# Kernel optimization log

Measured on AMD Instinct MI355X. Metric: run time of the kernel, lower is better.

Reference implementation:

```python
import jax, jax.numpy as jnp
import numpy as np

B, N, D = 8, 2048, 512


def setup_inputs() -> dict:
    key = jax.random.key(0)
    ks = jax.random.split(key, 8)
    s = 1.0 / np.sqrt(D)
    return {
        "x": jax.random.normal(ks[0], (B, N, D), dtype=jnp.float32),
        "event_lengths": jax.random.randint(ks[1], (B,), 1, N + 1, dtype=jnp.int64),
        "Wq": jax.random.uniform(ks[2], (D, D), jnp.float32, -s, s),
        "bq": jnp.zeros((D,), jnp.float32),
        "Wk": jax.random.uniform(ks[3], (D, D), jnp.float32, -s, s),
        "bk": jnp.zeros((D,), jnp.float32),
        "Wv": jax.random.uniform(ks[4], (D, D), jnp.float32, -s, s),
        "bv": jnp.zeros((D,), jnp.float32),
    }


def reference(x, event_lengths, Wq, bq, Wk, bk, Wv, bv):
    # x: [B, N, D]; linear layers follow torch convention y = x @ W^T + b
    q = jnp.einsum("bnd,ed->bne", x, Wq) + bq
    k = jnp.einsum("bnd,ed->bne", x, Wk) + bk
    v = jnp.einsum("bnd,ed->bne", x, Wv) + bv

    d = x.shape[-1]
    scores = jnp.einsum("bqd,bkd->bqk", q, k) / jnp.sqrt(jnp.asarray(d, jnp.float32))

    # per-sample padding mask: valid iff row < len AND col < len
    n = x.shape[1]
    idx = jnp.arange(n)
    L = event_lengths[:, None, None]  # [B,1,1]
    mask = (idx[None, :, None] < L) & (idx[None, None, :] < L)  # [B,N,N]
    scores = jnp.where(mask, scores, jnp.float32(-1e9))

    attn = jax.nn.softmax(scores, axis=-1)  # dropout omitted (eval mode)
    return jnp.einsum("bqk,bkd->bqd", attn, v)
```

## Files before the change

kernel.cpp:

```cpp
#include <hip/hip_runtime.h>

typedef _Float16 half8 __attribute__((ext_vector_type(8)));
typedef _Float16 half4 __attribute__((ext_vector_type(4)));
typedef float    floatx4 __attribute__((ext_vector_type(4)));
typedef float    float4v __attribute__((ext_vector_type(4)));

#define BB 8
#define NN 2048
#define DD 512


#define WAITV(N)  asm volatile("s_waitcnt vmcnt(" #N ")" ::: "memory")
#define WAITL0()  asm volatile("s_waitcnt lgkmcnt(0)" ::: "memory")
#define BARRIER() asm volatile("s_barrier" ::: "memory")

__device__ __forceinline__ void stage_tile(const _Float16* __restrict__ g,
                                           int gstride, _Float16* lds,
                                           int w, int lane)
{
#pragma unroll
    for (int j = 0; j < 2; ++j) {
        int grp = w * 2 + j;
        int r   = grp * 16 + (lane >> 2);
        int cb  = (lane & 3) ^ ((r >> 1) & 3);
        const _Float16* gp = g + (size_t)r * gstride + cb * 8;
        _Float16* lp = lds + grp * 512;
        __builtin_amdgcn_global_load_lds(
            (const __attribute__((address_space(1))) void*)gp,
            (__attribute__((address_space(3))) void*)lp, 16, 0, 0);
    }
}

__device__ __forceinline__ void stage_tile64(const _Float16* __restrict__ g,
                                             int gstride, _Float16* lds,
                                             int w, int lane)
{
    int r  = w * 16 + (lane >> 2);
    int cb = (lane & 3) ^ ((r >> 1) & 3);
    const _Float16* gp = g + (size_t)r * gstride + cb * 8;
    _Float16* lp = lds + w * 512;
    __builtin_amdgcn_global_load_lds(
        (const __attribute__((address_space(1))) void*)gp,
        (__attribute__((address_space(3))) void*)lp, 16, 0, 0);
}

__device__ __forceinline__ half8 frag(const _Float16* tile, int m, int quad)
{
    return *(const half8*)&tile[m * 32 + ((quad ^ ((m >> 1) & 3)) * 8)];
}

__global__ __launch_bounds__(256) void prep_kernel(
    const float* __restrict__ x, const float* __restrict__ Wq,
    const float* __restrict__ Wk, const float* __restrict__ Wv,
    const int* __restrict__ lens,
    _Float16* __restrict__ xh, _Float16* __restrict__ wqh,
    _Float16* __restrict__ wkh, _Float16* __restrict__ wvh)
{
    const int XQ = (BB * NN * DD) / 4;
    const int WQ = (DD * DD) / 4;
    int t = blockIdx.x * 256 + threadIdx.x;
    const float* src; _Float16* dst; int i;
    if (t < XQ) {
        int row = t >> 7;
        int b   = row >> 11;
        if ((row & 2047) >= ((lens[b] + 127) & ~127)) return;
        src = x;  dst = xh;  i = t;
    }
    else if (t < XQ + WQ)   { src = Wq; dst = wqh; i = t - XQ; }
    else if (t < XQ + 2*WQ) { src = Wk; dst = wkh; i = t - XQ - WQ; }
    else if (t < XQ + 3*WQ) { src = Wv; dst = wvh; i = t - XQ - 2*WQ; }
    else return;
    float4v f = *(const float4v*)&src[(size_t)i * 4];
    half4 h;
    for (int j = 0; j < 4; ++j) h[j] = (_Float16)f[j];
    *(half4*)&dst[(size_t)i * 4] = h;
}

__global__ __launch_bounds__(256) void meanx_kernel(
    const float* __restrict__ x, float* __restrict__ sx)
{
    const int b  = blockIdx.y;
    const int n0 = blockIdx.x * 64;
    const int d0 = threadIdx.x;
    float s0 = 0.f, s1 = 0.f;
    const float* base = x + ((size_t)b * NN + n0) * DD;
    for (int n = 0; n < 64; ++n) {
        s0 += base[n * DD + d0];
        s1 += base[n * DD + d0 + 256];
    }
    atomicAdd(&sx[b * DD + d0], s0);
    atomicAdd(&sx[b * DD + d0 + 256], s1);
}

__global__ __launch_bounds__(256) void mvgemv_kernel(
    const float* __restrict__ Wv, const float* __restrict__ bv,
    const float* __restrict__ sx, float* __restrict__ mean_v)
{
    const int blk = blockIdx.x;
    const int b   = blk >> 7;
    const int e   = (blk & 127) * 4 + (threadIdx.x >> 6);
    const int lane = threadIdx.x & 63;
    const float* wr = Wv + (size_t)e * DD + lane * 8;
    const float* xr = sx + b * DD + lane * 8;
    float s = 0.f;
    for (int j = 0; j < 8; ++j) s += wr[j] * xr[j];
    for (int off = 32; off > 0; off >>= 1) s += __shfl_xor(s, off);
    if (lane == 0)
        mean_v[b * DD + e] = s * (1.0f / 2048.0f) + bv[e];
}

__global__ __launch_bounds__(256) void projqk_kernel(
    const _Float16* __restrict__ xh,
    const _Float16* __restrict__ wqh, const _Float16* __restrict__ wkh,
    const float* __restrict__ bq, const float* __restrict__ bk,
    const int* __restrict__ lens,
    _Float16* __restrict__ qb, _Float16* __restrict__ kb)
{
    const int z = blockIdx.z;
    const int r0 = blockIdx.y * 128;
    const int bb = r0 >> 11;
    if ((r0 & 2047) >= lens[bb]) return;
    const _Float16* Wh  = z ? wkh : wqh;
    const float*    bias= z ? bk  : bq;
    _Float16*       outp= z ? kb  : qb;
    const int c0 = blockIdx.x * 128;

    __shared__ __align__(16) _Float16 As[3][128 * 32];
    __shared__ __align__(16) _Float16 Bs[3][128 * 32];

    const int tid  = threadIdx.x;
    const int lane = tid & 63;
    const int w    = tid >> 6;
    const int wm   = w >> 1, wn = w & 1;
    const int lr   = lane & 15;
    const int quad = lane >> 4;

    floatx4 zero; zero[0]=0.f; zero[1]=0.f; zero[2]=0.f; zero[3]=0.f;
    floatx4 acc[4][4];
    for (int i = 0; i < 4; ++i)
        for (int j = 0; j < 4; ++j) acc[i][j] = zero;

    const _Float16* Abase = xh + (size_t)r0 * DD;
    const _Float16* Bbase = Wh + (size_t)c0 * DD;

    stage_tile(Abase +  0, DD, As[0], w, lane);
    stage_tile(Bbase +  0, DD, Bs[0], w, lane);
    stage_tile(Abase + 32, DD, As[1], w, lane);
    stage_tile(Bbase + 32, DD, Bs[1], w, lane);

    int cur = 0;
    for (int kt = 0; kt < 16; ++kt) {
        int nx = (kt + 2 < 16) ? kt + 2 : 15;
        int nb = cur + 2; if (nb >= 3) nb -= 3;
        stage_tile(Abase + nx * 32, DD, As[nb], w, lane);
        stage_tile(Bbase + nx * 32, DD, Bs[nb], w, lane);
        WAITV(8);
        BARRIER();
        half8 a[4], b[4];
        for (int mt = 0; mt < 4; ++mt) a[mt] = frag(As[cur], wm * 64 + mt * 16 + lr, quad);
        for (int nt = 0; nt < 4; ++nt) b[nt] = frag(Bs[cur], wn * 64 + nt * 16 + lr, quad);
        for (int mt = 0; mt < 4; ++mt)
            for (int nt = 0; nt < 4; ++nt)
                acc[mt][nt] = __builtin_amdgcn_mfma_f32_16x16x32_f16(a[mt], b[nt], acc[mt][nt], 0, 0, 0);
        WAITL0();
        BARRIER();
        cur = (cur + 1 == 3) ? 0 : cur + 1;
    }
    WAITV(0);

    for (int mt = 0; mt < 4; ++mt)
        for (int nt = 0; nt < 4; ++nt)
            for (int r = 0; r < 4; ++r) {
                int row = r0 + wm * 64 + mt * 16 + quad * 4 + r;
                int col = c0 + wn * 64 + nt * 16 + lr;
                outp[(size_t)row * DD + col] = (_Float16)(acc[mt][nt][r] + bias[col]);
            }
}

__global__ __launch_bounds__(256) void projv_kernel(
    const _Float16* __restrict__ xh,
    const _Float16* __restrict__ wvh, const float* __restrict__ bv,
    const int* __restrict__ lens, _Float16* __restrict__ vhT)
{
    const int b  = blockIdx.z;
    const int e0 = blockIdx.y * 128;
    const int n0 = blockIdx.x * 128;
    if (n0 >= lens[b]) return;

    __shared__ __align__(16) _Float16 As[3][128 * 32];
    __shared__ __align__(16) _Float16 Bs[3][128 * 32];

    const int tid  = threadIdx.x;
    const int lane = tid & 63;
    const int w    = tid >> 6;
    const int wm   = w >> 1, wn = w & 1;
    const int lr   = lane & 15;
    const int quad = lane >> 4;

    floatx4 zero; zero[0]=0.f; zero[1]=0.f; zero[2]=0.f; zero[3]=0.f;
    floatx4 acc[4][4];
    for (int i = 0; i < 4; ++i)
        for (int j = 0; j < 4; ++j) acc[i][j] = zero;

    const _Float16* Abase = wvh + (size_t)e0 * DD;
    const _Float16* Bbase = xh + ((size_t)b * NN + n0) * DD;

    stage_tile(Abase +  0, DD, As[0], w, lane);
    stage_tile(Bbase +  0, DD, Bs[0], w, lane);
    stage_tile(Abase + 32, DD, As[1], w, lane);
    stage_tile(Bbase + 32, DD, Bs[1], w, lane);

    int cur = 0;
    for (int kt = 0; kt < 16; ++kt) {
        int nx = (kt + 2 < 16) ? kt + 2 : 15;
        int nb = cur + 2; if (nb >= 3) nb -= 3;
        stage_tile(Abase + nx * 32, DD, As[nb], w, lane);
        stage_tile(Bbase + nx * 32, DD, Bs[nb], w, lane);
        WAITV(8);
        BARRIER();
        half8 a[4], bfr[4];
        for (int mt = 0; mt < 4; ++mt) a[mt]   = frag(As[cur], wm * 64 + mt * 16 + lr, quad);
        for (int nt = 0; nt < 4; ++nt) bfr[nt] = frag(Bs[cur], wn * 64 + nt * 16 + lr, quad);
        for (int mt = 0; mt < 4; ++mt)
            for (int nt = 0; nt < 4; ++nt)
                acc[mt][nt] = __builtin_amdgcn_mfma_f32_16x16x32_f16(a[mt], bfr[nt], acc[mt][nt], 0, 0, 0);
        WAITL0();
        BARRIER();
        cur = (cur + 1 == 3) ? 0 : cur + 1;
    }
    WAITV(0);

    for (int mt = 0; mt < 4; ++mt)
        for (int nt = 0; nt < 4; ++nt)
            for (int r = 0; r < 4; ++r) {
                int e = e0 + wm * 64 + mt * 16 + quad * 4 + r;
                int n = n0 + wn * 64 + nt * 16 + lr;
                vhT[((size_t)b * DD + e) * NN + n] = (_Float16)(acc[mt][nt][r] + bv[e]);
            }
}

__global__ __launch_bounds__(256) void scores_kernel(
    const _Float16* __restrict__ qb, const _Float16* __restrict__ kb,
    const int* __restrict__ lens, _Float16* __restrict__ S)
{
    const int b  = blockIdx.z;
    const int r0 = blockIdx.y * 128;
    const int c0 = blockIdx.x * 128;
    const int L  = lens[b];
    if (r0 >= L || c0 >= L) return;
    const _Float16* Abase = qb + (size_t)b * NN * DD + (size_t)r0 * DD;
    const _Float16* Bbase = kb + (size_t)b * NN * DD + (size_t)c0 * DD;

    __shared__ __align__(16) _Float16 As[3][128 * 32];
    __shared__ __align__(16) _Float16 Bs[3][128 * 32];

    const int tid  = threadIdx.x;
    const int lane = tid & 63;
    const int w    = tid >> 6;
    const int wm   = w >> 1, wn = w & 1;
    const int lr   = lane & 15;
    const int quad = lane >> 4;

    floatx4 zero; zero[0]=0.f; zero[1]=0.f; zero[2]=0.f; zero[3]=0.f;
    floatx4 acc[4][4];
    for (int i = 0; i < 4; ++i)
        for (int j = 0; j < 4; ++j) acc[i][j] = zero;

    stage_tile(Abase +  0, DD, As[0], w, lane);
    stage_tile(Bbase +  0, DD, Bs[0], w, lane);
    stage_tile(Abase + 32, DD, As[1], w, lane);
    stage_tile(Bbase + 32, DD, Bs[1], w, lane);

    int cur = 0;
    for (int kt = 0; kt < 16; ++kt) {
        int nx = (kt + 2 < 16) ? kt + 2 : 15;
        int nb = cur + 2; if (nb >= 3) nb -= 3;
        stage_tile(Abase + nx * 32, DD, As[nb], w, lane);
        stage_tile(Bbase + nx * 32, DD, Bs[nb], w, lane);
        WAITV(8);
        BARRIER();
        half8 a[4], bfr[4];
        for (int mt = 0; mt < 4; ++mt) a[mt]   = frag(As[cur], wm * 64 + mt * 16 + lr, quad);
        for (int nt = 0; nt < 4; ++nt) bfr[nt] = frag(Bs[cur], wn * 64 + nt * 16 + lr, quad);
        for (int mt = 0; mt < 4; ++mt)
            for (int nt = 0; nt < 4; ++nt)
                acc[mt][nt] = __builtin_amdgcn_mfma_f32_16x16x32_f16(a[mt], bfr[nt], acc[mt][nt], 0, 0, 0);
        WAITL0();
        BARRIER();
        cur = (cur + 1 == 3) ? 0 : cur + 1;
    }
    WAITV(0);

    const float scale = 0.044194173824159216f;
    for (int mt = 0; mt < 4; ++mt)
        for (int nt = 0; nt < 4; ++nt)
            for (int r = 0; r < 4; ++r) {
                int q    = r0 + wm * 64 + mt * 16 + quad * 4 + r;
                int kcol = c0 + wn * 64 + nt * 16 + lr;
                S[((size_t)b * NN + q) * NN + kcol] = (_Float16)(acc[mt][nt][r] * scale);
            }
}

__global__ __launch_bounds__(256) void softmax_kernel(
    _Float16* __restrict__ S, const int* __restrict__ lens)
{
    const int b = blockIdx.y, q = blockIdx.x;
    const int L = lens[b];
    if (q >= L) return;
    const int Lp32 = (L + 31) & ~31;
    const size_t base = ((size_t)b * NN + q) * NN;
    const int tid  = threadIdx.x;
    const int lane = tid & 63;
    const int w    = tid >> 6;
    const int k0   = tid * 8;
    const bool active = k0 < Lp32;
    const float NEG = -__builtin_huge_valf();

    float f[8];
    if (active) {
        half8 v = *(const half8*)&S[base + k0];
        for (int j = 0; j < 8; ++j) f[j] = (k0 + j < L) ? (float)v[j] : NEG;
    } else {
        for (int j = 0; j < 8; ++j) f[j] = NEG;
    }

    float m = f[0];
    for (int j = 1; j < 8; ++j) m = fmaxf(m, f[j]);
    for (int off = 32; off > 0; off >>= 1) m = fmaxf(m, __shfl_xor(m, off));
    __shared__ float redm[4];
    __shared__ float reds[4];
    if (lane == 0) redm[w] = m;
    __syncthreads();
    m = fmaxf(fmaxf(redm[0], redm[1]), fmaxf(redm[2], redm[3]));

    float e[8], s = 0.f;
    for (int j = 0; j < 8; ++j) { e[j] = __expf(f[j] - m); s += e[j]; }
    for (int off = 32; off > 0; off >>= 1) s += __shfl_xor(s, off);
    if (lane == 0) reds[w] = s;
    __syncthreads();
    s = (reds[0] + reds[1]) + (reds[2] + reds[3]);

    float inv = 1.0f / s;
    if (active) {
        half8 o;
        for (int j = 0; j < 8; ++j) o[j] = (_Float16)(e[j] * inv);
        *(half8*)&S[base + k0] = o;
    }
}

__global__ __launch_bounds__(256) void pv_kernel(
    const _Float16* __restrict__ P, const _Float16* __restrict__ vhT,
    const int* __restrict__ lens, const float* __restrict__ mean_v,
    float* __restrict__ out)
{
    const int b  = blockIdx.z;
    const int L  = lens[b];
    const int r0 = blockIdx.y * 64;
    const int c0 = blockIdx.x * 128;
    const int KT = (r0 < L) ? ((L + 31) >> 5) : 0;
    const _Float16* A  = P   + (size_t)b * NN * NN + (size_t)r0 * NN;
    const _Float16* Vh = vhT + (size_t)b * DD * NN + (size_t)c0 * NN;

    __shared__ __align__(16) _Float16 As[4][64 * 32];
    __shared__ __align__(16) _Float16 Bhs[4][128 * 32];

    const int tid  = threadIdx.x;
    const int lane = tid & 63;
    const int w    = tid >> 6;
    const int lr   = lane & 15;
    const int quad = lane >> 4;

    floatx4 zero; zero[0]=0.f; zero[1]=0.f; zero[2]=0.f; zero[3]=0.f;
    floatx4 acc[4][2];
    for (int i = 0; i < 4; ++i)
        for (int j = 0; j < 2; ++j) acc[i][j] = zero;

    if (KT > 0) {
        for (int i = 0; i < 3; ++i) {
            int t0 = (i < KT) ? i : KT - 1;
            stage_tile64(A  + t0 * 32, NN, As[i],  w, lane);
            stage_tile (Vh + t0 * 32, NN, Bhs[i], w, lane);
        }
        int cur = 0;
        for (int kt = 0; kt < KT; ++kt) {
            int nx = (kt + 3 < KT) ? kt + 3 : KT - 1;
            int nb = cur + 3; if (nb >= 4) nb -= 4;
            stage_tile64(A  + nx * 32, NN, As[nb],  w, lane);
            stage_tile (Vh + nx * 32, NN, Bhs[nb], w, lane);
            WAITV(9);
            BARRIER();
            half8 a[4], bh[2];
            for (int mt = 0; mt < 4; ++mt) a[mt]  = frag(As[cur], mt * 16 + lr, quad);
            for (int nt = 0; nt < 2; ++nt) bh[nt] = frag(Bhs[cur], w * 32 + nt * 16 + lr, quad);
            for (int mt = 0; mt < 4; ++mt)
                for (int nt = 0; nt < 2; ++nt)
                    acc[mt][nt] = __builtin_amdgcn_mfma_f32_16x16x32_f16(a[mt], bh[nt], acc[mt][nt], 0, 0, 0);
            WAITL0();
            BARRIER();
            cur = (cur + 1 == 4) ? 0 : cur + 1;
        }
        WAITV(0);
    }

    float mval[2];
    for (int nt = 0; nt < 2; ++nt)
        mval[nt] = mean_v[b * DD + c0 + w * 32 + nt * 16 + lr];

    for (int mt = 0; mt < 4; ++mt)
        for (int nt = 0; nt < 2; ++nt)
            for (int r = 0; r < 4; ++r) {
                int q = r0 + mt * 16 + quad * 4 + r;
                int e = c0 + w * 32 + nt * 16 + lr;
                float val = (q < L) ? acc[mt][nt][r] : mval[nt];
                out[((size_t)b * NN + q) * DD + e] = val;
            }
}

extern "C" void kernel_launch(void* const* d_in, const int* in_sizes, int n_in,
                              void* d_out, int out_size, void* d_ws, size_t ws_size,
                              hipStream_t stream) {
    const float* x    = (const float*)d_in[0];
    const int*   lens = (const int*)d_in[1];
    const float* Wq   = (const float*)d_in[2];
    const float* bq   = (const float*)d_in[3];
    const float* Wk   = (const float*)d_in[4];
    const float* bk   = (const float*)d_in[5];
    const float* Wv   = (const float*)d_in[6];
    const float* bv   = (const float*)d_in[7];
    float* out = (float*)d_out;

    char* ws = (char*)d_ws;
    const size_t MB = 1024 * 1024;
    _Float16* qb  = (_Float16*)(ws);
    _Float16* kb  = (_Float16*)(ws + 16 * MB);
    _Float16* vh  = (_Float16*)(ws + 32 * MB);
    float*    mv  = (float*)   (ws + 48 * MB);
    float*    sx  = (float*)   (ws + 48 * MB + 64 * 1024);
    _Float16* S   = (_Float16*)(ws + 64 * MB);
    _Float16* xh  = (_Float16*)(ws + 64 * MB);
    _Float16* wqh = (_Float16*)(ws + 80 * MB);
    _Float16* wkh = (_Float16*)(ws + 80 * MB + 512 * 1024);
    _Float16* wvh = (_Float16*)(ws + 81 * MB);

    hipMemsetAsync(sx, 0, BB * DD * sizeof(float), stream);
    prep_kernel  <<<8960, 256, 0, stream>>>(x, Wq, Wk, Wv, lens, xh, wqh, wkh, wvh);
    meanx_kernel <<<dim3(32, 8),     256, 0, stream>>>(x, sx);
    mvgemv_kernel<<<1024,            256, 0, stream>>>(Wv, bv, sx, mv);
    projqk_kernel<<<dim3(4, 128, 2), 256, 0, stream>>>(xh, wqh, wkh, bq, bk, lens, qb, kb);
    projv_kernel <<<dim3(16, 4, 8),  256, 0, stream>>>(xh, wvh, bv, lens, vh);
    scores_kernel<<<dim3(16, 16, 8), 256, 0, stream>>>(qb, kb, lens, S);
    softmax_kernel<<<dim3(2048, 8),  256, 0, stream>>>(S, lens);
    pv_kernel    <<<dim3(4, 32, 8),  256, 0, stream>>>(S, vh, lens, mv, out);
}
```

Before: 211.6 us.

## Fuse softmax exponent into PV GEMM and merge mean-x with fp16 prep

Removes the standalone softmax pass. The PV kernel now exponentiates raw scores as it loads them from LDS, accumulates per-row sums, and divides at the epilogue. This skips a full read and write of the score matrix, but it also drops the max subtraction, so overflow safety depends on score magnitudes, and the exponentials are recomputed once per output column block. Separately, the x-to-fp16 conversion, the column sum of x and the weight casts are folded into one kernel. The PV pipeline is cut from four LDS buffers to a double buffer synchronised with __syncthreads.

```diff
diff --git a/kernel.cpp b/kernel.cpp
--- a/kernel.cpp
+++ b/kernel.cpp
@@ -1,9 +1,11 @@
 #include <hip/hip_runtime.h>
 
-typedef _Float16 half8 __attribute__((ext_vector_type(8)));
-typedef _Float16 half4 __attribute__((ext_vector_type(4)));
+typedef _Float16 half8  __attribute__((ext_vector_type(8)));
+typedef _Float16 half4  __attribute__((ext_vector_type(4)));
+typedef _Float16 half2v __attribute__((ext_vector_type(2)));
 typedef float    floatx4 __attribute__((ext_vector_type(4)));
 typedef float    float4v __attribute__((ext_vector_type(4)));
+typedef float    float2v __attribute__((ext_vector_type(2)));
 
 #define BB 8
 #define NN 2048
@@ -54,42 +56,47 @@
     const float* __restrict__ Wk, const float* __restrict__ Wv,
     const int* __restrict__ lens,
     _Float16* __restrict__ xh, _Float16* __restrict__ wqh,
-    _Float16* __restrict__ wkh, _Float16* __restrict__ wvh)
-{
-    const int XQ = (BB * NN * DD) / 4;
-    const int WQ = (DD * DD) / 4;
-    int t = blockIdx.x * 256 + threadIdx.x;
-    const float* src; _Float16* dst; int i;
-    if (t < XQ) {
-        int row = t >> 7;
-        int b   = row >> 11;
-        if ((row & 2047) >= ((lens[b] + 127) & ~127)) return;
-        src = x;  dst = xh;  i = t;
-    }
-    else if (t < XQ + WQ)   { src = Wq; dst = wqh; i = t - XQ; }
-    else if (t < XQ + 2*WQ) { src = Wk; dst = wkh; i = t - XQ - WQ; }
-    else if (t < XQ + 3*WQ) { src = Wv; dst = wvh; i = t - XQ - 2*WQ; }
-    else return;
-    float4v f = *(const float4v*)&src[(size_t)i * 4];
-    half4 h;
-    for (int j = 0; j < 4; ++j) h[j] = (_Float16)f[j];
-    *(half4*)&dst[(size_t)i * 4] = h;
-}
-
-__global__ __launch_bounds__(256) void meanx_kernel(
-    const float* __restrict__ x, float* __restrict__ sx)
+    _Float16* __restrict__ wkh, _Float16* __restrict__ wvh,
+    float* __restrict__ sx)
 {
     const int b  = blockIdx.y;
     const int n0 = blockIdx.x * 64;
-    const int d0 = threadIdx.x;
+    const int t  = threadIdx.x;
+    const int Lp = (lens[b] + 127) & ~127;
+    const float*   base  = x  + ((size_t)b * NN + n0) * DD + 2 * t;
+    _Float16*      hbase = xh + ((size_t)b * NN + n0) * DD + 2 * t;
+
+    int nw = Lp - n0;
+    nw = nw < 0 ? 0 : (nw > 64 ? 64 : nw);
+
     float s0 = 0.f, s1 = 0.f;
-    const float* base = x + ((size_t)b * NN + n0) * DD;
-    for (int n = 0; n < 64; ++n) {
-        s0 += base[n * DD + d0];
-        s1 += base[n * DD + d0 + 256];
-    }
-    atomicAdd(&sx[b * DD + d0], s0);
-    atomicAdd(&sx[b * DD + d0 + 256], s1);
+    int n = 0;
+    for (; n < nw; ++n) {
+        float2v f = *(const float2v*)&base[(size_t)n * DD];
+        s0 += f[0]; s1 += f[1];
+        half2v h; h[0] = (_Float16)f[0]; h[1] = (_Float16)f[1];
+        *(half2v*)&hbase[(size_t)n * DD] = h;
+    }
+    for (; n < 64; ++n) {
+        float2v f = *(const float2v*)&base[(size_t)n * DD];
+        s0 += f[0]; s1 += f[1];
+    }
+    atomicAdd(&sx[b * DD + 2 * t],     s0);
+    atomicAdd(&sx[b * DD + 2 * t + 1], s1);
+
+    const int gbid = b * 32 + blockIdx.x;
+#pragma unroll
+    for (int k = 0; k < 3; ++k) {
+        int wi = gbid * 768 + k * 256 + t;
+        const float* src; _Float16* dst; int i;
+        if (wi < 65536)       { src = Wq; dst = wqh; i = wi; }
+        else if (wi < 131072) { src = Wk; dst = wkh; i = wi - 65536; }
+        else                  { src = Wv; dst = wvh; i = wi - 131072; }
+        float4v f = *(const float4v*)&src[(size_t)i * 4];
+        half4 h;
+        for (int j = 0; j < 4; ++j) h[j] = (_Float16)f[j];
+        *(half4*)&dst[(size_t)i * 4] = h;
+    }
 }
 
 __global__ __launch_bounds__(256) void mvgemv_kernel(
@@ -301,55 +308,8 @@
             }
 }
 
-__global__ __launch_bounds__(256) void softmax_kernel(
-    _Float16* __restrict__ S, const int* __restrict__ lens)
-{
-    const int b = blockIdx.y, q = blockIdx.x;
-    const int L = lens[b];
-    if (q >= L) return;
-    const int Lp32 = (L + 31) & ~31;
-    const size_t base = ((size_t)b * NN + q) * NN;
-    const int tid  = threadIdx.x;
-    const int lane = tid & 63;
-    const int w    = tid >> 6;
-    const int k0   = tid * 8;
-    const bool active = k0 < Lp32;
-    const float NEG = -__builtin_huge_valf();
-
-    float f[8];
-    if (active) {
-        half8 v = *(const half8*)&S[base + k0];
-        for (int j = 0; j < 8; ++j) f[j] = (k0 + j < L) ? (float)v[j] : NEG;
-    } else {
-        for (int j = 0; j < 8; ++j) f[j] = NEG;
-    }
-
-    float m = f[0];
-    for (int j = 1; j < 8; ++j) m = fmaxf(m, f[j]);
-    for (int off = 32; off > 0; off >>= 1) m = fmaxf(m, __shfl_xor(m, off));
-    __shared__ float redm[4];
-    __shared__ float reds[4];
-    if (lane == 0) redm[w] = m;
-    __syncthreads();
-    m = fmaxf(fmaxf(redm[0], redm[1]), fmaxf(redm[2], redm[3]));
-
-    float e[8], s = 0.f;
-    for (int j = 0; j < 8; ++j) { e[j] = __expf(f[j] - m); s += e[j]; }
-    for (int off = 32; off > 0; off >>= 1) s += __shfl_xor(s, off);
-    if (lane == 0) reds[w] = s;
-    __syncthreads();
-    s = (reds[0] + reds[1]) + (reds[2] + reds[3]);
-
-    float inv = 1.0f / s;
-    if (active) {
-        half8 o;
-        for (int j = 0; j < 8; ++j) o[j] = (_Float16)(e[j] * inv);
-        *(half8*)&S[base + k0] = o;
-    }
-}
-
 __global__ __launch_bounds__(256) void pv_kernel(
-    const _Float16* __restrict__ P, const _Float16* __restrict__ vhT,
+    const _Float16* __restrict__ S, const _Float16* __restrict__ vhT,
     const int* __restrict__ lens, const float* __restrict__ mean_v,
     float* __restrict__ out)
 {
@@ -358,11 +318,11 @@
     const int r0 = blockIdx.y * 64;
     const int c0 = blockIdx.x * 128;
     const int KT = (r0 < L) ? ((L + 31) >> 5) : 0;
-    const _Float16* A  = P   + (size_t)b * NN * NN + (size_t)r0 * NN;
+    const _Float16* A  = S   + (size_t)b * NN * NN + (size_t)r0 * NN;
     const _Float16* Vh = vhT + (size_t)b * DD * NN + (size_t)c0 * NN;
 
-    __shared__ __align__(16) _Float16 As[4][64 * 32];
-    __shared__ __align__(16) _Float16 Bhs[4][128 * 32];
+    __shared__ __align__(16) _Float16 As[2][64 * 32];
+    __shared__ __align__(16) _Float16 Bhs[2][128 * 32];
 
     const int tid  = threadIdx.x;
     const int lane = tid & 63;
@@ -374,32 +334,45 @@
     floatx4 acc[4][2];
     for (int i = 0; i < 4; ++i)
         for (int j = 0; j < 2; ++j) acc[i][j] = zero;
+    float ls[4] = {0.f, 0.f, 0.f, 0.f};
 
     if (KT > 0) {
-        for (int i = 0; i < 3; ++i) {
-            int t0 = (i < KT) ? i : KT - 1;
-            stage_tile64(A  + t0 * 32, NN, As[i],  w, lane);
-            stage_tile (Vh + t0 * 32, NN, Bhs[i], w, lane);
+        stage_tile64(A, NN, As[0], w, lane);
+        stage_tile (Vh, NN, Bhs[0], w, lane);
+    }
+    for (int kt = 0; kt < KT; ++kt) {
+        const int cur = kt & 1;
+        __syncthreads();
+        if (kt + 1 < KT) {
+            stage_tile64(A + (size_t)(kt + 1) * 32, NN, As[cur ^ 1], w, lane);
+            stage_tile (Vh + (size_t)(kt + 1) * 32, NN, Bhs[cur ^ 1], w, lane);
         }
-        int cur = 0;
-        for (int kt = 0; kt < KT; ++kt) {
-            int nx = (kt + 3 < KT) ? kt + 3 : KT - 1;
-            int nb = cur + 3; if (nb >= 4) nb -= 4;
-            stage_tile64(A  + nx * 32, NN, As[nb],  w, lane);
-            stage_tile (Vh + nx * 32, NN, Bhs[nb], w, lane);
-            WAITV(9);
-            BARRIER();
-            half8 a[4], bh[2];
-            for (int mt = 0; mt < 4; ++mt) a[mt]  = frag(As[cur], mt * 16 + lr, quad);
-            for (int nt = 0; nt < 2; ++nt) bh[nt] = frag(Bhs[cur], w * 32 + nt * 16 + lr, quad);
-            for (int mt = 0; mt < 4; ++mt)
-                for (int nt = 0; nt < 2; ++nt)
-                    acc[mt][nt] = __builtin_amdgcn_mfma_f32_16x16x32_f16(a[mt], bh[nt], acc[mt][nt], 0, 0, 0);
-            WAITL0();
-            BARRIER();
-            cur = (cur + 1 == 4) ? 0 : cur + 1;
+        const int kbase = kt * 32 + quad * 8;
+        half8 a[4], bh[2];
+#pragma unroll
+        for (int mt = 0; mt < 4; ++mt) {
+            half8 sraw = frag(As[cur], mt * 16 + lr, quad);
+            half8 p;
+            float lsum = 0.f;
+#pragma unroll
+            for (int j = 0; j < 8; ++j) {
+                float e = (kbase + j < L) ? __expf((float)sraw[j]) : 0.f;
+                lsum += e;
+                p[j] = (_Float16)e;
+            }
+            ls[mt] += lsum;
+            a[mt] = p;
         }
-        WAITV(0);
+        for (int nt = 0; nt < 2; ++nt) bh[nt] = frag(Bhs[cur], w * 32 + nt * 16 + lr, quad);
+        for (int mt = 0; mt < 4; ++mt)
+            for (int nt = 0; nt < 2; ++nt)
+                acc[mt][nt] = __builtin_amdgcn_mfma_f32_16x16x32_f16(a[mt], bh[nt], acc[mt][nt], 0, 0, 0);
+    }
+
+#pragma unroll
+    for (int mt = 0; mt < 4; ++mt) {
+        ls[mt] += __shfl_xor(ls[mt], 16);
+        ls[mt] += __shfl_xor(ls[mt], 32);
     }
 
     float mval[2];
@@ -407,13 +380,16 @@
         mval[nt] = mean_v[b * DD + c0 + w * 32 + nt * 16 + lr];
 
     for (int mt = 0; mt < 4; ++mt)
-        for (int nt = 0; nt < 2; ++nt)
-            for (int r = 0; r < 4; ++r) {
-                int q = r0 + mt * 16 + quad * 4 + r;
+        for (int r = 0; r < 4; ++r) {
+            int q = r0 + mt * 16 + quad * 4 + r;
+            float denom = __shfl(ls[mt], quad * 4 + r);
+            float inv = 1.0f / denom;
+            for (int nt = 0; nt < 2; ++nt) {
                 int e = c0 + w * 32 + nt * 16 + lr;
-                float val = (q < L) ? acc[mt][nt][r] : mval[nt];
+                float val = (q < L) ? acc[mt][nt][r] * inv : mval[nt];
                 out[((size_t)b * NN + q) * DD + e] = val;
             }
+        }
 }
 
 extern "C" void kernel_launch(void* const* d_in, const int* in_sizes, int n_in,
@@ -443,12 +419,10 @@
     _Float16* wvh = (_Float16*)(ws + 81 * MB);
 
     hipMemsetAsync(sx, 0, BB * DD * sizeof(float), stream);
-    prep_kernel  <<<8960, 256, 0, stream>>>(x, Wq, Wk, Wv, lens, xh, wqh, wkh, wvh);
-    meanx_kernel <<<dim3(32, 8),     256, 0, stream>>>(x, sx);
+    prep_kernel  <<<dim3(32, 8),     256, 0, stream>>>(x, Wq, Wk, Wv, lens, xh, wqh, wkh, wvh, sx);
     mvgemv_kernel<<<1024,            256, 0, stream>>>(Wv, bv, sx, mv);
     projqk_kernel<<<dim3(4, 128, 2), 256, 0, stream>>>(xh, wqh, wkh, bq, bk, lens, qb, kb);
     projv_kernel <<<dim3(16, 4, 8),  256, 0, stream>>>(xh, wvh, bv, lens, vh);
     scores_kernel<<<dim3(16, 16, 8), 256, 0, stream>>>(qb, kb, lens, S);
-    softmax_kernel<<<dim3(2048, 8),  256, 0, stream>>>(S, lens);
     pv_kernel    <<<dim3(4, 32, 8),  256, 0, stream>>>(S, vh, lens, mv, out);
 }
```

New measurement: 267.2 us. 26.3% more time.
